# Kernel optimization log

Measured on AMD Instinct MI355X. Metric: run time of the kernel, lower is better.

## Reference

```python
import jax, jax.numpy as jnp
import numpy as np

T, B, D_IN = 1024, 64, 17
H_MAIN = 150   # per-direction hidden of main bi-GRU (hidden_dim=300)
H_HIER = 128   # per-direction hidden of hier bi-GRU (hier_hidden=256)
M = 16         # uniform measure length (eoM fires every M steps)
N_MEAS = T // M
N_PITCH, N_KS = 35, 15
PAD_P, PAD_K = 34, 14


def _gru(x, Wih, Whh, bih, bhh):
    # x: [T, N, D]; torch GRU gate order is (r, z, n)
    H = Whh.shape[1]
    gi_all = jnp.einsum('tnd,gd->tng', x, Wih) + bih  # input-side gates, precomputed

    def step(h, gi):
        gh = h @ Whh.T + bhh
        ir, iz, inn = jnp.split(gi, 3, axis=-1)
        hr, hz, hn = jnp.split(gh, 3, axis=-1)
        r = jax.nn.sigmoid(ir + hr)
        z = jax.nn.sigmoid(iz + hz)
        n = jnp.tanh(inn + r * hn)
        h_new = (1.0 - z) * n + z * h
        return h_new, h_new

    h0 = jnp.zeros((x.shape[1], H), x.dtype)
    _, ys = jax.lax.scan(step, h0, gi_all)
    return ys


def _bigru(x, pf, pb):
    yf = _gru(x, *pf)
    yb = _gru(x[::-1], *pb)[::-1]
    return jnp.concatenate([yf, yb], axis=-1)


def _ce(logits, targets, pad_idx):
    # mean cross-entropy with ignore_index=pad_idx
    logp = jax.nn.log_softmax(logits, axis=-1)
    mask = (targets != pad_idx).astype(logits.dtype)
    nll = -jnp.take_along_axis(logp, targets[:, None], axis=1)[:, 0]
    return jnp.sum(nll * mask) / jnp.maximum(jnp.sum(mask), 1.0)


def _forward(sentences, mWih_f, mWhh_f, mbih_f, mbhh_f, mWih_b, mWhh_b, mbih_b, mbhh_b,
             hWih_f, hWhh_f, hbih_f, hbhh_f, hWih_b, hWhh_b, hbih_b, hbhh_b,
             Wq, bq, Wv, bv, Wp, bp, Wk, bk, pitches, keysignatures):
    # main bi-GRU over full sequences: [T, B, 300]
    rnn_out = _bigru(sentences, (mWih_f, mWhh_f, mbih_f, mbhh_f),
                     (mWih_b, mWhh_b, mbih_b, mbhh_b))
    H2 = rnn_out.shape[-1]
    # carve uniform measures: [T,B,H2] -> [M, B*N_MEAS, H2]
    seg = rnn_out.reshape(N_MEAS, M, B, H2).transpose(1, 2, 0, 3).reshape(M, B * N_MEAS, H2)
    hier = _bigru(seg, (hWih_f, hWhh_f, hbih_f, hbhh_f),
                  (hWih_b, hWhh_b, hbih_b, hbhh_b))  # [M, B*N_MEAS, 256]
    HH = hier.shape[-1]
    # attention per measure: query = value = hier outputs [B*N_MEAS, M, 256]
    hv = hier.reshape(M, B, N_MEAS, HH).transpose(1, 2, 0, 3).reshape(B * N_MEAS, M, HH)
    q = hv @ Wq.T + bq
    v = hv @ Wv.T + bv
    attn = jax.nn.softmax(jnp.einsum('nld,nmd->nlm', q, v), axis=-1)
    ctx = jnp.einsum('nlm,nmd->nd', attn, hv).reshape(B, N_MEAS, HH)  # sum over l of attn@value
    # repeat each measure context over its M timesteps: [T, B, 256]
    ctx_t = jnp.repeat(ctx, M, axis=1).transpose(1, 0, 2)
    stacked = jnp.concatenate([rnn_out, ctx_t], axis=-1)  # [T, B, 556]
    out_pitch = stacked @ Wp.T + bp   # [T, B, 35]
    out_ks = ctx_t @ Wk.T + bk        # [T, B, 15]
    return (_ce(out_pitch.reshape(-1, N_PITCH), pitches.reshape(-1), PAD_P)
            + _ce(out_ks.reshape(-1, N_KS), keysignatures.reshape(-1), PAD_K))


def setup_inputs() -> dict:
    key = jax.random.key(0)
    ks = jax.random.split(key, 32)

    def w(i, *shape):
        return jax.random.normal(ks[i], shape, jnp.float32) * 0.05

    G_M, G_H = 3 * H_MAIN, 3 * H_HIER
    inp = {
        'sentences': jax.random.normal(ks[0], (T, B, D_IN), jnp.float32),
        'pitches': jax.random.randint(ks[1], (T, B), 0, PAD_P),
        'keysignatures': jax.random.randint(ks[2], (T, B), 0, PAD_K),
        'sentences_len': jnp.full((B,), T, dtype=jnp.int32),
        'eoM': jnp.tile(((jnp.arange(T) % M) == M - 1).astype(jnp.int32)[:, None], (1, B)),
        'mWih_f': w(3, G_M, D_IN), 'mWhh_f': w(4, G_M, H_MAIN), 'mbih_f': w(5, G_M), 'mbhh_f': w(6, G_M),
        'mWih_b': w(7, G_M, D_IN), 'mWhh_b': w(8, G_M, H_MAIN), 'mbih_b': w(9, G_M), 'mbhh_b': w(10, G_M),
        'hWih_f': w(11, G_H, 2 * H_MAIN), 'hWhh_f': w(12, G_H, H_HIER), 'hbih_f': w(13, G_H), 'hbhh_f': w(14, G_H),
        'hWih_b': w(15, G_H, 2 * H_MAIN), 'hWhh_b': w(16, G_H, H_HIER), 'hbih_b': w(17, G_H), 'hbhh_b': w(18, G_H),
        'Wq': w(19, 2 * H_HIER, 2 * H_HIER), 'bq': w(20, 2 * H_HIER),
        'Wv': w(21, 2 * H_HIER, 2 * H_HIER), 'bv': w(22, 2 * H_HIER),
        'Wp': w(23, N_PITCH, 2 * H_MAIN + 2 * H_HIER), 'bp': w(24, N_PITCH),
        'Wk': w(25, N_KS, 2 * H_HIER), 'bk': w(26, N_KS),
    }
    return inp


def reference(sentences, pitches, keysignatures, sentences_len, eoM,
              mWih_f, mWhh_f, mbih_f, mbhh_f, mWih_b, mWhh_b, mbih_b, mbhh_b,
              hWih_f, hWhh_f, hbih_f, hbhh_f, hWih_b, hWhh_b, hbih_b, hbhh_b,
              Wq, bq, Wv, bv, Wp, bp, Wk, bk):
    # sentences_len/eoM encode the (uniform) measure structure M=16, full lengths;
    # the segment layout is baked in statically, so they are structural constants here.
    return _forward(sentences, mWih_f, mWhh_f, mbih_f, mbhh_f, mWih_b, mWhh_b, mbih_b, mbhh_b,
                    hWih_f, hWhh_f, hbih_f, hbhh_f, hWih_b, hWhh_b, hbih_b, hbhh_b,
                    Wq, bq, Wv, bv, Wp, bp, Wk, bk, pitches, keysignatures)
```

## Files before the change

kernel.cpp:

```cpp
#include <hip/hip_runtime.h>
#include <cstddef>

constexpr int kT   = 1024;
constexpr int kB   = 64;
constexpr int kDIN = 17;
constexpr int kHM  = 150;
constexpr int kHH  = 128;
constexpr int kM   = 16;
constexpr int kD2  = 300;
constexpr int kNP  = 35;
constexpr int kNK  = 15;

constexpr size_t OFF_RNN16  = 0;
constexpr size_t OFF_HV16   = 10485760;
constexpr size_t OFF_PTPACK = 19988480;
constexpr size_t OFF_U      = 20021248;
constexpr size_t OFF_W      = 20021504;
constexpr size_t OFF_C0     = 20021760;
constexpr size_t OFF_ACC    = 20021776;
constexpr size_t OFF_KSLOGP = 20021792;
constexpr size_t OFF_CLOG   = 20083232;
constexpr size_t OFF_BPACK  = 20318752;
constexpr size_t OFF_BPACKL = 20490784;

typedef __bf16 bf16x8 __attribute__((ext_vector_type(8)));
typedef float f32x4 __attribute__((ext_vector_type(4)));

__device__ __forceinline__ unsigned short f2bf(float f) {
  unsigned u = __float_as_uint(f);
  u += 0x7FFFu + ((u >> 16) & 1u);
  return (unsigned short)(u >> 16);
}
__device__ __forceinline__ float bf2f(unsigned short v) {
  return __uint_as_float(((unsigned)v) << 16);
}
__device__ __forceinline__ float sigm(float x) {
  return __builtin_amdgcn_rcpf(1.f + __expf(-x));
}
__device__ __forceinline__ float tanh_fast(float x) {
  return 1.f - 2.f * __builtin_amdgcn_rcpf(__expf(2.f * x) + 1.f);
}

__global__ __launch_bounds__(640, 2) void k_mega(
    const float* __restrict__ x,
    const float* __restrict__ mWih_f, const float* __restrict__ mWhh_f,
    const float* __restrict__ mWih_b, const float* __restrict__ mWhh_b,
    const float* __restrict__ mbih_f, const float* __restrict__ mbhh_f,
    const float* __restrict__ mbih_b, const float* __restrict__ mbhh_b,
    const float* __restrict__ hWih_f, const float* __restrict__ hWhh_f,
    const float* __restrict__ hWih_b, const float* __restrict__ hWhh_b,
    const float* __restrict__ Wp,
    const float* __restrict__ Wq, const float* __restrict__ bq,
    const float* __restrict__ Wv, const float* __restrict__ bv,
    unsigned short* __restrict__ rnn16,
    unsigned short* __restrict__ bpack,
    unsigned short* __restrict__ bpackL,
    unsigned short* __restrict__ pp,
    float* __restrict__ u, float* __restrict__ w,
    float* __restrict__ c0, float* __restrict__ acc)
{
  __shared__ __align__(16) unsigned short hx[2][160];
  __shared__ __align__(16) unsigned short hist[2][16][160];
  __shared__ __align__(16) unsigned short xall[kT][32];
  const int blk = blockIdx.x;
  if (blk < 128) {
    const int d = blk & 1, b = blk >> 1;
    const int tid = threadIdx.x, wv = tid >> 6, lane = tid & 63;
    const int col = lane & 15, q8 = (lane >> 4) * 8;
    for (int i = tid; i < 2 * 160; i += 640) ((unsigned short*)hx)[i] = 0;
    for (int i = tid; i < 2 * 16 * 160; i += 640) ((unsigned short*)hist)[i] = 0;
    for (int i = tid; i < kT * 32; i += 640) {
      const int t = i >> 5, c = i & 31;
      xall[t][c] = (c < kDIN) ? f2bf(x[((size_t)t * kB + b) * kDIN + c]) : (unsigned short)0;
    }
    const float* bih = d ? mbih_b : mbih_f;
    const float* bhh = d ? mbhh_b : mbhh_f;
    const float* Wihd = d ? mWih_b : mWih_f;
    const float* Whhd = d ? mWhh_b : mWhh_f;
    const int j = wv * 16 + col;
    const bool actv = (lane < 16) && (j < kHM);
    float br = 0.f, bz = 0.f, bnx = 0.f, bnh = 0.f;
    if (actv) {
      br  = bih[j] + bhh[j];
      bz  = bih[150 + j] + bhh[150 + j];
      bnx = bih[300 + j];
      bnh = bhh[300 + j];
    }
    bf16x8 bw[3][6];
    const int gts[3] = { wv, 10 + wv, 20 + wv };
#pragma unroll
    for (int gi = 0; gi < 3; gi++) {
      const int slot = gts[gi] * 16 + col;
      const int type = slot / 160, jh = slot - type * 160;
      const int row = type * 150 + jh;
      const bool valid = (jh < 150);
#pragma unroll
      for (int kt = 0; kt < 6; kt++) {
        union { bf16x8 v; unsigned short us[8]; } tmp;
#pragma unroll
        for (int jj = 0; jj < 8; jj++) {
          float f = 0.f;
          if (valid) {
            if (kt < 5) {
              const int k = kt * 32 + (lane >> 4) * 8 + jj;
              if (k < 150) f = Whhd[row * 150 + k];
            } else {
              const int k = (lane >> 4) * 8 + jj;
              if (k < 17) f = Wihd[row * 17 + k];
            }
          }
          tmp.us[jj] = f2bf(f);
        }
        bw[gi][kt] = tmp.v;
      }
    }
    float h_old = 0.f;
    __syncthreads();

    for (int t = 0; t < kT; t++) {
      const int tx = d ? (kT - 1 - t) : t;
      const int buf = t & 1;
      bf16x8 afr[6];
#pragma unroll
      for (int kt = 0; kt < 5; kt++) afr[kt] = *(const bf16x8*)&hx[buf][kt * 32 + q8];
      afr[5] = *(const bf16x8*)&xall[tx][q8];
      f32x4 aR0 = (f32x4)(0.f), aR1 = (f32x4)(0.f);
      f32x4 aZ0 = (f32x4)(0.f), aZ1 = (f32x4)(0.f);
      f32x4 aN0 = (f32x4)(0.f), aN1 = (f32x4)(0.f);
      f32x4 aX  = (f32x4)(0.f);
#pragma unroll
      for (int kt = 0; kt < 6; kt++) {
        const bf16x8 af = afr[kt];
        if ((kt & 1) == 0) {
          aR0 = __builtin_amdgcn_mfma_f32_16x16x32_bf16(af, bw[0][kt], aR0, 0, 0, 0);
          aZ0 = __builtin_amdgcn_mfma_f32_16x16x32_bf16(af, bw[1][kt], aZ0, 0, 0, 0);
          aN0 = __builtin_amdgcn_mfma_f32_16x16x32_bf16(af, bw[2][kt], aN0, 0, 0, 0);
        } else if (kt < 5) {
          aR1 = __builtin_amdgcn_mfma_f32_16x16x32_bf16(af, bw[0][kt], aR1, 0, 0, 0);
          aZ1 = __builtin_amdgcn_mfma_f32_16x16x32_bf16(af, bw[1][kt], aZ1, 0, 0, 0);
          aN1 = __builtin_amdgcn_mfma_f32_16x16x32_bf16(af, bw[2][kt], aN1, 0, 0, 0);
        } else {
          aR1 = __builtin_amdgcn_mfma_f32_16x16x32_bf16(af, bw[0][5], aR1, 0, 0, 0);
          aZ1 = __builtin_amdgcn_mfma_f32_16x16x32_bf16(af, bw[1][5], aZ1, 0, 0, 0);
          aX  = __builtin_amdgcn_mfma_f32_16x16x32_bf16(af, bw[2][5], aX, 0, 0, 0);
        }
      }
      if (actv) {
        const float r = sigm(aR0[0] + aR1[0] + br);
        const float z = sigm(aZ0[0] + aZ1[0] + bz);
        const float n = tanh_fast(aX[0] + bnx + r * (aN0[0] + aN1[0] + bnh));
        h_old = (1.f - z) * n + z * h_old;
        const unsigned short us = f2bf(h_old);
        hx[buf ^ 1][j] = us;
        hist[(t >> 4) & 1][t & 15][j] = us;
      }
      __syncthreads();
      if ((t & 15) == 15) {
        const int hb = (t >> 4) & 1;
        const int toff = tid / 40, ch = tid - toff * 40;
        const int tg = t - 15 + toff;
        const int txg = d ? (kT - 1 - tg) : tg;
        *(ushort4*)&rnn16[((size_t)txg * kB + b) * 320 + d * 160 + ch * 4] =
            *(const ushort4*)&hist[hb][toff][ch * 4];
      }
    }
  } else if (blk < 199) {
    const int sub = threadIdx.x >> 6, lane = threadIdx.x & 63;
    int bid = (blk - 128) * 10 + sub;
    if (bid >= 702) return;
    if (bid < 672) {
      const int kt = bid % 14;
      const int nt = (bid / 14) % 24;
      const int d  = bid / (14 * 24);
      const float* Wih = d ? hWih_b : hWih_f;
      const float* Whh = d ? hWhh_b : hWhh_f;
      const int n = nt * 16 + (lane & 15);
      const int kbase = kt * 32 + (lane >> 4) * 8;
      unsigned short* dst = bpack + ((((size_t)d * 24 + nt) * 14 + kt) * 64 + lane) * 8;
#pragma unroll
      for (int jj = 0; jj < 8; jj++) {
        const int k = kbase + jj;
        float f = 0.f;
        if (kt < 10) {
          if (k < 150) f = Wih[n * 300 + k];
          else if (k >= 160 && k < 310) f = Wih[n * 300 + (k - 10)];
        } else {
          f = Whh[n * 128 + (k - 320)];
        }
        dst[jj] = f2bf(f);
      }
    } else {
      bid -= 672;
      const int kt = bid % 10, nt = bid / 10;
      const int n = nt * 16 + (lane & 15);
      const int kbase = kt * 32 + (lane >> 4) * 8;
      unsigned short* dst = bpackL + (((size_t)bid) * 64 + lane) * 8;
#pragma unroll
      for (int jj = 0; jj < 8; jj++) {
        const int k = kbase + jj;
        float f = 0.f;
        if (n < kNP) {
          if (k < 150) f = Wp[n * 556 + k];
          else if (k >= 160 && k < 310) f = Wp[n * 556 + (k - 10)];
        }
        dst[jj] = f2bf(f);
      }
    }
  } else if (blk < 212) {
    const int sub = threadIdx.x >> 6, lane = threadIdx.x & 63;
    const int bid = (blk - 199) * 10 + sub;
    if (bid >= 128) return;
    const int kt = bid & 7, nt = bid >> 3;
    const int c = nt * 16 + (lane & 15);
    const int e0 = kt * 32 + (lane >> 4) * 8;
    float av[8];
#pragma unroll
    for (int jj = 0; jj < 8; jj++) av[jj] = 0.f;
    for (int a = 0; a < 256; a++) {
      const float wq = Wq[a * 256 + c];
#pragma unroll
      for (int jj = 0; jj < 8; jj++) av[jj] += wq * Wv[a * 256 + e0 + jj];
    }
    unsigned short* dst = pp + ((size_t)bid * 64 + lane) * 8;
#pragma unroll
    for (int jj = 0; jj < 8; jj++) dst[jj] = f2bf(av[jj]);
  } else {
    const int a = threadIdx.x;
    if (a >= 256) return;
    float us = 0.f, ws = 0.f;
    for (int jj = 0; jj < 256; jj++) {
      us += Wq[jj * 256 + a] * bv[jj];
      ws += bq[jj] * Wv[jj * 256 + a];
    }
    u[a] = us; w[a] = ws;
    if (a == 0) {
      float cc = 0.f;
      for (int jj = 0; jj < 256; jj++) cc += bq[jj] * bv[jj];
      c0[0] = cc;
      acc[0] = acc[1] = acc[2] = acc[3] = acc[4] = 0.f;
    }
  }
}

__global__ __launch_bounds__(512, 1) void k_hier_mfma(
    const unsigned short* __restrict__ rnn16,
    const unsigned short* __restrict__ bpack,
    const float* __restrict__ bihf, const float* __restrict__ bhhf,
    const float* __restrict__ bihb, const float* __restrict__ bhhb,
    unsigned short* __restrict__ hv16)
{
  const int d = blockIdx.x & 1;
  const int bn0 = (blockIdx.x >> 1) * 16;
  const int tid = threadIdx.x;
  const int w = tid >> 6;
  const int lane = tid & 63;
  const int q = lane >> 4, col = lane & 15, q8 = q * 8;

  __shared__ __align__(16) unsigned short x_s[2][16][328];
  __shared__ __align__(16) unsigned short h_s[16][136];

  for (int i = tid; i < 16 * 136; i += 512) ((unsigned short*)h_s)[i] = 0;
  const float* bih = d ? bihb : bihf;
  const float* bhh = d ? bhhb : bhhf;
  const int j = w * 16 + col;
  const float biR  = bih[j] + bhh[j];
  const float biZ  = bih[128 + j] + bhh[128 + j];
  const float biNX = bih[256 + j];
  const float biNH = bhh[256 + j];
  float h32r[4] = {0.f, 0.f, 0.f, 0.f};

  bf16x8 bw[3][14];
  const unsigned short* bpd = bpack + (size_t)d * 24 * 14 * 64 * 8;
  const int nts[3] = { w, 8 + w, 16 + w };
#pragma unroll
  for (int gi = 0; gi < 3; gi++)
#pragma unroll
    for (int kt = 0; kt < 14; kt++)
      bw[gi][kt] = *(const bf16x8*)&bpd[(((size_t)nts[gi] * 14 + kt) * 64 + lane) * 8];

  {
    const int mx0 = d ? 15 : 0;
    for (int i = tid; i < 640; i += 512) {
      const int r = i / 40, c = i - r * 40;
      const int bn = bn0 + r, bb = bn >> 6, nn = bn & 63;
      *(uint4*)&x_s[0][r][c * 8] =
          *(const uint4*)&rnn16[((size_t)(nn * 16 + mx0) * 64 + bb) * 320 + c * 8];
    }
  }
  __syncthreads();

  for (int m = 0; m < kM; m++) {
    const int mx = d ? (15 - m) : m;
    const int buf = m & 1;
    f32x4 aR = (f32x4)(0.f), aZ = (f32x4)(0.f), aNX = (f32x4)(0.f), aNH = (f32x4)(0.f);
#pragma unroll
    for (int kt = 0; kt < 14; kt++) {
      const bf16x8 af = (kt < 10) ? *(const bf16x8*)&x_s[buf][col][kt * 32 + q8]
                                  : *(const bf16x8*)&h_s[col][(kt - 10) * 32 + q8];
      aR = __builtin_amdgcn_mfma_f32_16x16x32_bf16(af, bw[0][kt], aR, 0, 0, 0);
      aZ = __builtin_amdgcn_mfma_f32_16x16x32_bf16(af, bw[1][kt], aZ, 0, 0, 0);
      if (kt < 10) aNX = __builtin_amdgcn_mfma_f32_16x16x32_bf16(af, bw[2][kt], aNX, 0, 0, 0);
      else         aNH = __builtin_amdgcn_mfma_f32_16x16x32_bf16(af, bw[2][kt], aNH, 0, 0, 0);
    }
    __syncthreads();
#pragma unroll
    for (int i = 0; i < 4; i++) {
      const int row = q * 4 + i;
      const float rr = sigm(aR[i] + biR);
      const float zz = sigm(aZ[i] + biZ);
      const float nn2 = tanh_fast(aNX[i] + biNX + rr * (aNH[i] + biNH));
      const float hnew = (1.f - zz) * nn2 + zz * h32r[i];
      h32r[i] = hnew;
      const unsigned short us = f2bf(hnew);
      h_s[row][j] = us;
      hv16[((size_t)(bn0 + row) * kM + mx) * 256 + d * kHH + j] = us;
    }
    if (m + 1 < kM) {
      const int mxn = d ? (15 - (m + 1)) : (m + 1);
      for (int i = tid; i < 640; i += 512) {
        const int r = i / 40, c = i - r * 40;
        const int bn = bn0 + r, bb = bn >> 6, nn = bn & 63;
        *(uint4*)&x_s[buf ^ 1][r][c * 8] =
            *(const uint4*)&rnn16[((size_t)(nn * 16 + mxn) * 64 + bb) * 320 + c * 8];
      }
    }
    __syncthreads();
  }
}

__global__ __launch_bounds__(256) void k_attn_ctx(
    const unsigned short* __restrict__ hv16, const unsigned short* __restrict__ ptpack,
    const float* __restrict__ u, const float* __restrict__ w,
    const float* __restrict__ c0p,
    const float* __restrict__ Wp, const float* __restrict__ bp,
    const float* __restrict__ Wk, const float* __restrict__ bk,
    float* __restrict__ clog, float* __restrict__ kslogp) {
  const int tid = threadIdx.x;
  const int wv = tid >> 6, lane = tid & 63, col = lane & 15, q = lane >> 4, q8 = q * 8;
  __shared__ __align__(16) unsigned short hv16s[16][264];
  __shared__ __align__(16) unsigned short Ts16[16][264];
  __shared__ __align__(16) float W2[50][260];
  __shared__ __align__(16) float cs[256];
  __shared__ __align__(16) float us[256], wss[256];
  __shared__ float pu[16][17], pw[16][17];
  __shared__ float uh[16], wh[16], SM[16];
  __shared__ float As[16][17];
  __shared__ float arr[64];
  __shared__ float bps[35], bks[15];
  const float c0 = c0p[0];
  for (int i = tid; i < 35 * 256; i += 256) { const int r = i >> 8, c = i & 255; W2[r][c] = Wp[r * 556 + 300 + c]; }
  for (int i = tid; i < 15 * 256; i += 256) { const int r = i >> 8, c = i & 255; W2[35 + r][c] = Wk[r * 256 + c]; }
  us[tid] = u[tid];
  wss[tid] = w[tid];
  if (tid < 35) bps[tid] = bp[tid];
  else if (tid < 50) bks[tid - 35] = bk[tid - 35];
  bf16x8 bpt[4][8];
#pragma unroll
  for (int i2 = 0; i2 < 4; i2++)
#pragma unroll
    for (int kt = 0; kt < 8; kt++)
      bpt[i2][kt] = *(const bf16x8*)&ptpack[((((size_t)(wv * 4 + i2)) * 8 + kt) * 64 + lane) * 8];

  const int srow = tid >> 4, sci = (tid & 15) * 16;
  {
    const unsigned short* src = hv16 + (size_t)(blockIdx.x * 8) * 4096;
#pragma unroll
    for (int k = 0; k < 16; k += 4)
      *(ushort4*)&hv16s[srow][sci + k] = *(const ushort4*)&src[srow * 256 + sci + k];
  }
  __syncthreads();

  for (int ni = 0; ni < 8; ni++) {
    const int n = blockIdx.x * 8 + ni;
    ushort4 pf[4];
    if (ni + 1 < 8) {
      const unsigned short* src = hv16 + (size_t)(n + 1) * 4096;
#pragma unroll
      for (int k2 = 0; k2 < 4; k2++) pf[k2] = *(const ushort4*)&src[srow * 256 + sci + k2 * 4];
    }
    {
      f32x4 acc4[4];
#pragma unroll
      for (int i2 = 0; i2 < 4; i2++) acc4[i2] = (f32x4)(0.f);
#pragma unroll
      for (int kt = 0; kt < 8; kt++) {
        const bf16x8 af = *(const bf16x8*)&hv16s[col][kt * 32 + q8];
#pragma unroll
        for (int i2 = 0; i2 < 4; i2++)
          acc4[i2] = __builtin_amdgcn_mfma_f32_16x16x32_bf16(af, bpt[i2][kt], acc4[i2], 0, 0, 0);
      }
#pragma unroll
      for (int i2 = 0; i2 < 4; i2++) {
        const int nt = wv * 4 + i2;
#pragma unroll
        for (int i = 0; i < 4; i++) Ts16[q * 4 + i][nt * 16 + col] = f2bf(acc4[i2][i]);
      }
    }
    {
      const int l = tid >> 4, s = tid & 15;
      float su = 0.f, sw = 0.f;
#pragma unroll
      for (int a0 = 0; a0 < 16; a0++) {
        const int a = s * 16 + a0;
        const float hvv = bf2f(hv16s[l][a]);
        su += hvv * us[a];
        sw += hvv * wss[a];
      }
      pu[l][s] = su; pw[l][s] = sw;
    }
    __syncthreads();
    if (tid < 16) { float s2 = 0.f; for (int s = 0; s < 16; s++) s2 += pu[tid][s]; uh[tid] = s2; }
    else if (tid < 32) { float s2 = 0.f; for (int s = 0; s < 16; s++) s2 += pw[tid - 16][s]; wh[tid - 16] = s2; }
    __syncthreads();
    if (tid < 64) {
      f32x4 sa = (f32x4)(0.f);
#pragma unroll
      for (int kt = 0; kt < 8; kt++) {
        const bf16x8 af  = *(const bf16x8*)&hv16s[col][kt * 32 + q8];
        const bf16x8 bts = *(const bf16x8*)&Ts16[col][kt * 32 + q8];
        sa = __builtin_amdgcn_mfma_f32_16x16x32_bf16(af, bts, sa, 0, 0, 0);
      }
#pragma unroll
      for (int i = 0; i < 4; i++) {
        const int l = q * 4 + i;
        float sc = sa[i] + c0 + uh[l] + wh[col];
        float mxv = sc;
#pragma unroll
        for (int o = 8; o >= 1; o >>= 1) mxv = fmaxf(mxv, __shfl_xor(mxv, o, 16));
        const float e = __expf(sc - mxv);
        float se = e;
#pragma unroll
        for (int o = 8; o >= 1; o >>= 1) se += __shfl_xor(se, o, 16);
        As[l][col] = e / se;
      }
    }
    __syncthreads();
    if (tid < 16) {
      float s = 0.f;
      for (int l2 = 0; l2 < 16; l2++) s += As[l2][tid];
      SM[tid] = s;
    }
    __syncthreads();
    {
      float cv = 0.f;
#pragma unroll
      for (int m2 = 0; m2 < 16; m2++) cv += SM[m2] * bf2f(hv16s[m2][tid]);
      cs[tid] = cv;
    }
    __syncthreads();
    if (ni + 1 < 8) {
#pragma unroll
      for (int k2 = 0; k2 < 4; k2++) *(ushort4*)&hv16s[srow][sci + k2 * 4] = pf[k2];
    }
    {
      const int o = tid >> 2, s = tid & 3;
      float v = 0.f;
      if (o < 50) {
        for (int k0 = 0; k0 < 64; k0 += 4) {
          const int k = s * 64 + k0;
          const float4 wq = *(const float4*)&W2[o][k];
          const float4 cq = *(const float4*)&cs[k];
          v += wq.x * cq.x + wq.y * cq.y + wq.z * cq.z + wq.w * cq.w;
        }
      }
      v += __shfl_xor(v, 1);
      v += __shfl_xor(v, 2);
      if (o < 50 && s == 0) arr[o] = v;
    }
    __syncthreads();
    if (tid < 35) clog[n * kNP + tid] = arr[tid] + bps[tid];
    if (tid >= 64 && tid < 80) {
      const int t2 = tid - 64;
      float kk = (t2 < 15) ? arr[35 + t2] + bks[t2] : -1e30f;
      float mxv = kk;
#pragma unroll
      for (int off = 8; off >= 1; off >>= 1) mxv = fmaxf(mxv, __shfl_xor(mxv, off, 16));
      const float e = (t2 < 15) ? __expf(kk - mxv) : 0.f;
      float se = e;
#pragma unroll
      for (int off = 8; off >= 1; off >>= 1) se += __shfl_xor(se, off, 16);
      if (t2 < 15) kslogp[n * kNK + t2] = kk - mxv - __logf(se);
    }
    __syncthreads();
  }
}

__global__ __launch_bounds__(256, 2) void k_loss_mfma(
    const unsigned short* __restrict__ rnn16,
    const unsigned short* __restrict__ bpackL,
    const float* __restrict__ clog,
    const float* __restrict__ ks_logp,
    const int* __restrict__ pitches, const int* __restrict__ kss,
    float* __restrict__ acc, float* __restrict__ out) {
  const int tid = threadIdx.x, w = tid >> 6, lane = tid & 63;
  const int col = lane & 15, q = lane >> 4, q8 = q * 8;
  bf16x8 bl[3][10];
#pragma unroll
  for (int nt = 0; nt < 3; nt++)
#pragma unroll
    for (int kt = 0; kt < 10; kt++)
      bl[nt][kt] = *(const bf16x8*)&bpackL[(((size_t)nt * 10 + kt) * 64 + lane) * 8];

  float sp = 0.f, cp = 0.f, sk = 0.f, ck = 0.f;
#pragma unroll
  for (int mt = 0; mt < 2; mt++) {
    const int rowbase = blockIdx.x * 128 + w * 32 + mt * 16;
    f32x4 a0 = (f32x4)(0.f), a1 = (f32x4)(0.f), a2 = (f32x4)(0.f);
#pragma unroll
    for (int kt = 0; kt < 10; kt++) {
      const bf16x8 af = *(const bf16x8*)&rnn16[(size_t)(rowbase + col) * 320 + kt * 32 + q8];
      a0 = __builtin_amdgcn_mfma_f32_16x16x32_bf16(af, bl[0][kt], a0, 0, 0, 0);
      a1 = __builtin_amdgcn_mfma_f32_16x16x32_bf16(af, bl[1][kt], a1, 0, 0, 0);
      a2 = __builtin_amdgcn_mfma_f32_16x16x32_bf16(af, bl[2][kt], a2, 0, 0, 0);
    }
#pragma unroll
    for (int i = 0; i < 4; i++) {
      const int row = rowbase + q * 4 + i;
      const int t = row >> 6, b = row & 63;
      const int bn = b * 64 + (t >> 4);
      const float lg0 = a0[i] + clog[bn * kNP + col];
      const float lg1 = a1[i] + clog[bn * kNP + 16 + col];
      const float lg2 = (col < 3) ? (a2[i] + clog[bn * kNP + 32 + col]) : -1e30f;
      float mx = fmaxf(fmaxf(lg0, lg1), lg2);
#pragma unroll
      for (int o = 8; o >= 1; o >>= 1) mx = fmaxf(mx, __shfl_xor(mx, o, 16));
      float se = __expf(lg0 - mx) + __expf(lg1 - mx) + __expf(lg2 - mx);
#pragma unroll
      for (int o = 8; o >= 1; o >>= 1) se += __shfl_xor(se, o, 16);
      const int tp = pitches[row];
      const float cand = (tp < 16) ? a0[i] : (tp < 32) ? a1[i] : a2[i];
      const float tva = __shfl(cand, (lane & 48) | (tp & 15), 64);
      if (col == 0 && tp != 34) {
        sp += (mx + __logf(se)) - (tva + clog[bn * kNP + tp]);
        cp += 1.f;
      }
      if (col == 1) {
        const int tk = kss[row];
        if (tk != 14) { sk -= ks_logp[bn * kNK + tk]; ck += 1.f; }
      }
    }
  }
#pragma unroll
  for (int o = 32; o >= 1; o >>= 1) {
    sp += __shfl_xor(sp, o, 64);
    cp += __shfl_xor(cp, o, 64);
    sk += __shfl_xor(sk, o, 64);
    ck += __shfl_xor(ck, o, 64);
  }
  if (lane == 0) {
    atomicAdd(&acc[0], sp); atomicAdd(&acc[1], cp);
    atomicAdd(&acc[2], sk); atomicAdd(&acc[3], ck);
  }
  __syncthreads();
  if (tid == 0) {
    __threadfence();
    const float done = atomicAdd(&acc[4], 1.f);
    if (done == (float)(gridDim.x - 1)) {
      const float a0 = atomicAdd(&acc[0], 0.f);
      const float a1 = atomicAdd(&acc[1], 0.f);
      const float a2 = atomicAdd(&acc[2], 0.f);
      const float a3 = atomicAdd(&acc[3], 0.f);
      out[0] = a0 / fmaxf(a1, 1.f) + a2 / fmaxf(a3, 1.f);
    }
  }
}

extern "C" void kernel_launch(void* const* d_in, const int* in_sizes, int n_in,
                              void* d_out, int out_size, void* d_ws, size_t ws_size,
                              hipStream_t stream) {
  (void)in_sizes; (void)n_in; (void)out_size; (void)ws_size;
  const float* sent    = (const float*)d_in[0];
  const int*   pitches = (const int*)d_in[1];
  const int*   kss     = (const int*)d_in[2];
  const float* mWih_f  = (const float*)d_in[5];
  const float* mWhh_f  = (const float*)d_in[6];
  const float* mbih_f  = (const float*)d_in[7];
  const float* mbhh_f  = (const float*)d_in[8];
  const float* mWih_b  = (const float*)d_in[9];
  const float* mWhh_b  = (const float*)d_in[10];
  const float* mbih_b  = (const float*)d_in[11];
  const float* mbhh_b  = (const float*)d_in[12];
  const float* hWih_f  = (const float*)d_in[13];
  const float* hWhh_f  = (const float*)d_in[14];
  const float* hbih_f  = (const float*)d_in[15];
  const float* hbhh_f  = (const float*)d_in[16];
  const float* hWih_b  = (const float*)d_in[17];
  const float* hWhh_b  = (const float*)d_in[18];
  const float* hbih_b  = (const float*)d_in[19];
  const float* hbhh_b  = (const float*)d_in[20];
  const float* Wq      = (const float*)d_in[21];
  const float* bq      = (const float*)d_in[22];
  const float* Wv      = (const float*)d_in[23];
  const float* bv      = (const float*)d_in[24];
  const float* Wp      = (const float*)d_in[25];
  const float* bp      = (const float*)d_in[26];
  const float* Wk      = (const float*)d_in[27];
  const float* bk      = (const float*)d_in[28];
  float* ws  = (float*)d_ws;
  float* out = (float*)d_out;
  unsigned short* rnn16  = (unsigned short*)(ws + OFF_RNN16);
  unsigned short* hv16   = (unsigned short*)(ws + OFF_HV16);
  unsigned short* ptpack = (unsigned short*)(ws + OFF_PTPACK);
  unsigned short* bpackL = (unsigned short*)(ws + OFF_BPACKL);
  unsigned short* bpack  = (unsigned short*)(ws + OFF_BPACK);

  k_mega<<<213, 640, 0, stream>>>(sent,
                                  mWih_f, mWhh_f, mWih_b, mWhh_b,
                                  mbih_f, mbhh_f, mbih_b, mbhh_b,
                                  hWih_f, hWhh_f, hWih_b, hWhh_b, Wp,
                                  Wq, bq, Wv, bv,
                                  rnn16, bpack, bpackL, ptpack,
                                  ws + OFF_U, ws + OFF_W, ws + OFF_C0, ws + OFF_ACC);
  k_hier_mfma<<<512, 512, 0, stream>>>(rnn16, bpack,
                                       hbih_f, hbhh_f, hbih_b, hbhh_b, hv16);
  k_attn_ctx<<<512, 256, 0, stream>>>(hv16, ptpack, ws + OFF_U, ws + OFF_W,
                                      ws + OFF_C0, Wp, bp, Wk, bk,
                                      ws + OFF_CLOG, ws + OFF_KSLOGP);
  k_loss_mfma<<<512, 256, 0, stream>>>(rnn16, bpackL, ws + OFF_CLOG, ws + OFF_KSLOGP,
                                       pitches, kss, ws + OFF_ACC, out);
}
```

Measured before the change: 1.025 ms.

## Split main GRU recurrence into two launches and prefetch hier inputs into registers

Runs the sequential main bi-GRU in two kernel launches over time halves, saving the hidden state to workspace between them and converting only the needed half of the input per launch. Weight packing is vectorised with float2 loads. In the hier kernel, the next step's rnn16 tile is loaded into registers before the MFMA loop and stored to shared memory afterwards, so global load latency overlaps compute. The split adds an extra launch and state round-trip. It keeps the serial dependency, so the recurrence is not shortened.

Result: no change. 1.026 ms (+0.1%).

```diff
diff --git a/kernel.cpp b/kernel.cpp
--- a/kernel.cpp
+++ b/kernel.cpp
@@ -13,6 +13,7 @@
 
 constexpr size_t OFF_RNN16  = 0;
 constexpr size_t OFF_HV16   = 10485760;
+constexpr size_t OFF_HSAVE  = 18874368;
 constexpr size_t OFF_PTPACK = 19988480;
 constexpr size_t OFF_U      = 20021248;
 constexpr size_t OFF_W      = 20021504;
@@ -57,7 +58,9 @@
     unsigned short* __restrict__ bpackL,
     unsigned short* __restrict__ pp,
     float* __restrict__ u, float* __restrict__ w,
-    float* __restrict__ c0, float* __restrict__ acc)
+    float* __restrict__ c0, float* __restrict__ acc,
+    float* __restrict__ hsave,
+    int t_begin, int t_end)
 {
   __shared__ __align__(16) unsigned short hx[2][160];
   __shared__ __align__(16) unsigned short hist[2][16][160];
@@ -69,9 +72,13 @@
     const int col = lane & 15, q8 = (lane >> 4) * 8;
     for (int i = tid; i < 2 * 160; i += 640) ((unsigned short*)hx)[i] = 0;
     for (int i = tid; i < 2 * 16 * 160; i += 640) ((unsigned short*)hist)[i] = 0;
-    for (int i = tid; i < kT * 32; i += 640) {
-      const int t = i >> 5, c = i & 31;
-      xall[t][c] = (c < kDIN) ? f2bf(x[((size_t)t * kB + b) * kDIN + c]) : (unsigned short)0;
+    {
+      const int rlo = d ? (kT - t_end) : t_begin;
+      for (int i = tid; i < 512 * 32; i += 640) {
+        const int tt = rlo + (i >> 5), c = i & 31;
+        xall[tt][c] = (c < kDIN) ? f2bf(x[((size_t)tt * kB + b) * kDIN + c])
+                                 : (unsigned short)0;
+      }
     }
     const float* bih = d ? mbih_b : mbih_f;
     const float* bhh = d ? mbhh_b : mbhh_f;
@@ -88,6 +95,7 @@
     }
     bf16x8 bw[3][6];
     const int gts[3] = { wv, 10 + wv, 20 + wv };
+    const int kb = (lane >> 4) * 8;
 #pragma unroll
     for (int gi = 0; gi < 3; gi++) {
       const int slot = gts[gi] * 16 + col;
@@ -97,27 +105,42 @@
 #pragma unroll
       for (int kt = 0; kt < 6; kt++) {
         union { bf16x8 v; unsigned short us[8]; } tmp;
-#pragma unroll
-        for (int jj = 0; jj < 8; jj++) {
-          float f = 0.f;
-          if (valid) {
-            if (kt < 5) {
-              const int k = kt * 32 + (lane >> 4) * 8 + jj;
-              if (k < 150) f = Whhd[row * 150 + k];
-            } else {
-              const int k = (lane >> 4) * 8 + jj;
-              if (k < 17) f = Wihd[row * 17 + k];
+        if (kt < 5) {
+          const int k0 = kt * 32 + kb;
+          if (valid && (k0 + 8 <= 150)) {
+#pragma unroll
+            for (int p = 0; p < 4; p++) {
+              const float2 f2 = *(const float2*)&Whhd[row * 150 + k0 + 2 * p];
+              tmp.us[2 * p]     = f2bf(f2.x);
+              tmp.us[2 * p + 1] = f2bf(f2.y);
+            }
+          } else {
+#pragma unroll
+            for (int jj = 0; jj < 8; jj++) {
+              const int k = k0 + jj;
+              tmp.us[jj] = (valid && k < 150) ? f2bf(Whhd[row * 150 + k])
+                                              : (unsigned short)0;
             }
           }
-          tmp.us[jj] = f2bf(f);
+        } else {
+#pragma unroll
+          for (int jj = 0; jj < 8; jj++) {
+            const int k = kb + jj;
+            tmp.us[jj] = (valid && k < 17) ? f2bf(Wihd[row * 17 + k])
+                                           : (unsigned short)0;
+          }
         }
         bw[gi][kt] = tmp.v;
       }
     }
     float h_old = 0.f;
-    __syncthreads();
-
-    for (int t = 0; t < kT; t++) {
+    if (t_begin > 0 && actv) {
+      h_old = hsave[blk * 160 + j];
+      hx[t_begin & 1][j] = f2bf(h_old);
+    }
+    __syncthreads();
+
+    for (int t = t_begin; t < t_end; t++) {
       const int tx = d ? (kT - 1 - t) : t;
       const int buf = t & 1;
       bf16x8 afr[6];
@@ -164,6 +187,7 @@
             *(const ushort4*)&hist[hb][toff][ch * 4];
       }
     }
+    if (t_end < kT && actv) hsave[blk * 160 + j] = h_old;
   } else if (blk < 199) {
     const int sub = threadIdx.x >> 6, lane = threadIdx.x & 63;
     int bid = (blk - 128) * 10 + sub;
@@ -278,20 +302,32 @@
     for (int kt = 0; kt < 14; kt++)
       bw[gi][kt] = *(const bf16x8*)&bpd[(((size_t)nts[gi] * 14 + kt) * 64 + lane) * 8];
 
+  const int i0 = tid,        r0 = i0 / 40, c0 = i0 - r0 * 40;
+  const int i1 = tid + 512,  r1 = i1 / 40, c1 = i1 - r1 * 40;
+  const int bnA = bn0 + r0, bbA = bnA >> 6, nnA = bnA & 63;
+  const int bnB = bn0 + r1, bbB = bnB >> 6, nnB = bnB & 63;
+
   {
     const int mx0 = d ? 15 : 0;
-    for (int i = tid; i < 640; i += 512) {
-      const int r = i / 40, c = i - r * 40;
-      const int bn = bn0 + r, bb = bn >> 6, nn = bn & 63;
-      *(uint4*)&x_s[0][r][c * 8] =
-          *(const uint4*)&rnn16[((size_t)(nn * 16 + mx0) * 64 + bb) * 320 + c * 8];
-    }
+    *(uint4*)&x_s[0][r0][c0 * 8] =
+        *(const uint4*)&rnn16[((size_t)(nnA * 16 + mx0) * 64 + bbA) * 320 + c0 * 8];
+    if (tid < 128)
+      *(uint4*)&x_s[0][r1][c1 * 8] =
+          *(const uint4*)&rnn16[((size_t)(nnB * 16 + mx0) * 64 + bbB) * 320 + c1 * 8];
   }
   __syncthreads();
 
   for (int m = 0; m < kM; m++) {
     const int mx = d ? (15 - m) : m;
     const int buf = m & 1;
+    uint4 pf0, pf1;
+    const bool has = (m + 1 < kM);
+    if (has) {
+      const int mxn = d ? (15 - (m + 1)) : (m + 1);
+      pf0 = *(const uint4*)&rnn16[((size_t)(nnA * 16 + mxn) * 64 + bbA) * 320 + c0 * 8];
+      if (tid < 128)
+        pf1 = *(const uint4*)&rnn16[((size_t)(nnB * 16 + mxn) * 64 + bbB) * 320 + c1 * 8];
+    }
     f32x4 aR = (f32x4)(0.f), aZ = (f32x4)(0.f), aNX = (f32x4)(0.f), aNH = (f32x4)(0.f);
 #pragma unroll
     for (int kt = 0; kt < 14; kt++) {
@@ -315,14 +351,9 @@
       h_s[row][j] = us;
       hv16[((size_t)(bn0 + row) * kM + mx) * 256 + d * kHH + j] = us;
     }
-    if (m + 1 < kM) {
-      const int mxn = d ? (15 - (m + 1)) : (m + 1);
-      for (int i = tid; i < 640; i += 512) {
-        const int r = i / 40, c = i - r * 40;
-        const int bn = bn0 + r, bb = bn >> 6, nn = bn & 63;
-        *(uint4*)&x_s[buf ^ 1][r][c * 8] =
-            *(const uint4*)&rnn16[((size_t)(nn * 16 + mxn) * 64 + bb) * 320 + c * 8];
-      }
+    if (has) {
+      *(uint4*)&x_s[buf ^ 1][r0][c0 * 8] = pf0;
+      if (tid < 128) *(uint4*)&x_s[buf ^ 1][r1][c1 * 8] = pf1;
     }
     __syncthreads();
   }
@@ -603,6 +634,7 @@
   unsigned short* ptpack = (unsigned short*)(ws + OFF_PTPACK);
   unsigned short* bpackL = (unsigned short*)(ws + OFF_BPACKL);
   unsigned short* bpack  = (unsigned short*)(ws + OFF_BPACK);
+  float* hsave = ws + OFF_HSAVE;
 
   k_mega<<<213, 640, 0, stream>>>(sent,
                                   mWih_f, mWhh_f, mWih_b, mWhh_b,
@@ -610,7 +642,16 @@
                                   hWih_f, hWhh_f, hWih_b, hWhh_b, Wp,
                                   Wq, bq, Wv, bv,
                                   rnn16, bpack, bpackL, ptpack,
-                                  ws + OFF_U, ws + OFF_W, ws + OFF_C0, ws + OFF_ACC);
+                                  ws + OFF_U, ws + OFF_W, ws + OFF_C0, ws + OFF_ACC,
+                                  hsave, 0, 512);
+  k_mega<<<128, 640, 0, stream>>>(sent,
+                                  mWih_f, mWhh_f, mWih_b, mWhh_b,
+                                  mbih_f, mbhh_f, mbih_b, mbhh_b,
+                                  hWih_f, hWhh_f, hWih_b, hWhh_b, Wp,
+                                  Wq, bq, Wv, bv,
+                                  rnn16, bpack, bpackL, ptpack,
+                                  ws + OFF_U, ws + OFF_W, ws + OFF_C0, ws + OFF_ACC,
+                                  hsave, 512, 1024);
   k_hier_mfma<<<512, 512, 0, stream>>>(rnn16, bpack,
                                        hbih_f, hbhh_f, hbih_b, hbhh_b, hv16);
   k_attn_ctx<<<512, 256, 0, stream>>>(hv16, ptpack, ws + OFF_U, ws + OFF_W,
```
